# Kernel optimization log

Hardware: AMD Instinct MI355X
Metric: run time of the kernel (lower is better)

The kernel has to match this reference:

```python
import jax, jax.numpy as jnp
import numpy as np

HIDDEN = 2048
H = 16            # num heads
Q_RANK = 1536
KV_RANK = 512
D_NOPE = 128
D_ROPE = 64
D_QK = D_NOPE + D_ROPE   # 192
D_V = 128
ROPE_BASE = 10000.0
EPS = 1e-6


def _rms_norm(x, w):
    xf = x.astype(jnp.float32)
    var = jnp.mean(xf * xf, axis=-1, keepdims=True)
    return w * (xf * jax.lax.rsqrt(var + EPS)).astype(x.dtype)


def _rotate_half(x):
    x1, x2 = x[..., : x.shape[-1] // 2], x[..., x.shape[-1] // 2:]
    return jnp.concatenate((-x2, x1), axis=-1)


def _rope_cos_sin(position_ids, dtype):
    inv_freq = 1.0 / (ROPE_BASE ** (jnp.arange(0, D_ROPE, 2, dtype=jnp.float32) / D_ROPE))
    freqs = position_ids.astype(jnp.float32)[..., None] * inv_freq  # [b,s,32]
    emb = jnp.concatenate((freqs, freqs), axis=-1)                  # [b,s,64]
    return jnp.cos(emb).astype(dtype), jnp.sin(emb).astype(dtype)


def setup_inputs() -> dict:
    key = jax.random.key(0)
    ks = jax.random.split(key, 8)
    b, s = 1, 2048
    scale = 0.02
    return {
        "hidden_states": jax.random.normal(ks[0], (b, s, HIDDEN), jnp.float32),
        "position_ids": jnp.broadcast_to(jnp.arange(s, dtype=jnp.int64)[None, :], (b, s)),
        "q_a_w": jax.random.normal(ks[1], (Q_RANK, HIDDEN), jnp.float32) * scale,
        "q_a_ln_w": jnp.ones((Q_RANK,), jnp.float32),
        "q_b_w": jax.random.normal(ks[2], (H * D_QK, Q_RANK), jnp.float32) * scale,
        "kv_a_w": jax.random.normal(ks[3], (KV_RANK + D_ROPE, HIDDEN), jnp.float32) * scale,
        "kv_a_ln_w": jnp.ones((KV_RANK,), jnp.float32),
        "kv_b_w": jax.random.normal(ks[4], (H * (D_NOPE + D_V), KV_RANK), jnp.float32) * scale,
        "o_w": jax.random.normal(ks[5], (HIDDEN, H * D_V), jnp.float32) * scale,
    }


def reference(hidden_states, position_ids, q_a_w, q_a_ln_w, q_b_w, kv_a_w, kv_a_ln_w, kv_b_w, o_w):
    b, s, _ = hidden_states.shape
    softmax_scale = D_QK ** (-0.5)

    # Q path: low-rank down-proj -> RMSNorm -> up-proj
    q_a = hidden_states @ q_a_w.T                              # [b,s,q_rank]
    q = (_rms_norm(q_a, q_a_ln_w) @ q_b_w.T).reshape(b, s, H, D_QK)
    q_nope, q_pe = q[..., :D_NOPE], q[..., D_NOPE:]

    # KV path: joint down-proj -> split latent / rope part
    kv_a = hidden_states @ kv_a_w.T                            # [b,s,kv_rank+rope]
    compressed_kv = _rms_norm(kv_a[..., :KV_RANK], kv_a_ln_w)  # [b,s,kv_rank]
    k_pe = kv_a[..., KV_RANK:]                                 # [b,s,rope]
    kv_b = (compressed_kv @ kv_b_w.T).reshape(b, s, H, D_NOPE + D_V)
    k_nope, v = kv_b[..., :D_NOPE], kv_b[..., D_NOPE:]

    # decoupled RoPE on the rope slice
    cos, sin = _rope_cos_sin(position_ids, hidden_states.dtype)  # [b,s,64]
    cos, sin = cos[:, :, None, :], sin[:, :, None, :]            # [b,s,1,64]
    q_pe = q_pe * cos + _rotate_half(q_pe) * sin                 # [b,s,H,64]
    k_pe_h = jnp.broadcast_to(k_pe[:, :, None, :], (b, s, H, D_ROPE))
    k_pe_h = k_pe_h * cos + _rotate_half(k_pe_h) * sin

    q_full = jnp.concatenate([q_nope, q_pe], axis=-1)            # [b,s,H,192]
    k_full = jnp.concatenate([k_nope, k_pe_h], axis=-1)          # [b,s,H,192]

    # naive materialized attention (matches reference)
    scores = jnp.einsum("bqhd,bkhd->bhqk", q_full, k_full) * softmax_scale
    causal = jnp.triu(jnp.full((s, s), -jnp.inf, dtype=scores.dtype), k=1)
    scores = scores + causal
    probs = jax.nn.softmax(scores.astype(jnp.float32), axis=-1).astype(q_full.dtype)
    attn = jnp.einsum("bhqk,bkhd->bqhd", probs, v).reshape(b, s, H * D_V)
    return attn @ o_w.T
```

## Files before the change

kernel.cpp:

```cpp
#include <hip/hip_runtime.h>
#include <stdint.h>

#define S_LEN 2048
#define HIDDEN_ 2048
#define NH 16
#define QR 1536
#define KVR 512
#define DN 128
#define DR 64
#define DQK 192
#define DV 128
#define NQKV 2112

#define KT_STRIDE 6144
#define VT_STRIDE 4096

typedef __attribute__((ext_vector_type(8))) short bf16x8;
typedef __attribute__((ext_vector_type(4))) float f32x4;
typedef __attribute__((ext_vector_type(4))) unsigned short u16x4;
typedef unsigned short u16;
typedef unsigned int u32;

#define GLOAD_LDS16(g, l)                                                      \
    __builtin_amdgcn_global_load_lds(                                          \
        (const __attribute__((address_space(1))) void*)(g),                    \
        (__attribute__((address_space(3))) void*)(l), 16, 0, 0)

__device__ inline float bf2f(u16 x) {
    union { u32 u; float f; } v; v.u = ((u32)x) << 16; return v.f;
}
__device__ inline u16 f2bf(float f) {
    union { float f; u32 u; } v; v.f = f;
    u32 u = v.u;
    return (u16)((u + 0x7fffu + ((u >> 16) & 1u)) >> 16);
}

__global__ void cvt_multi(const float* s0, u16* d0, int n0,
                          const float* s1, u16* d1, int n1,
                          const float* s2, u16* d2, int n2,
                          const float* s3, u16* d3, int n3,
                          const float* s4, u16* d4, int n4,
                          const float* s5, u16* d5, int n5)
{
    const float* src; u16* dst; int n;
    switch (blockIdx.y) {
        case 0: src = s0; dst = d0; n = n0; break;
        case 1: src = s1; dst = d1; n = n1; break;
        case 2: src = s2; dst = d2; n = n2; break;
        case 3: src = s3; dst = d3; n = n3; break;
        case 4: src = s4; dst = d4; n = n4; break;
        default: src = s5; dst = d5; n = n5; break;
    }
    int i = (blockIdx.x * 256 + threadIdx.x) * 4;
    if (i + 3 < n) {
        float4 v = *(const float4*)(src + i);
        u16x4 o;
        o[0] = f2bf(v.x); o[1] = f2bf(v.y); o[2] = f2bf(v.z); o[3] = f2bf(v.w);
        *(u16x4*)(dst + i) = o;
    }
}

__device__ __forceinline__
void gemm_body(const u16* __restrict__ A, const u16* __restrict__ B,
               void* __restrict__ Cv, int M, int N, int Kloop, int ld,
               int out_f32, int bx, int by)
{
    __shared__ u16 sA[128 * 32];
    __shared__ u16 sB[128 * 32];
    const int tid  = threadIdx.x;
    const int wave = tid >> 6;
    const int lane = tid & 63;
    const int l16  = lane & 15;
    const int quad = lane >> 4;
    const int m_blk = by * 128;
    const int n_blk = bx * 128;
    const int wm = (wave >> 1) * 64;
    const int wn = (wave & 1) * 64;

    const f32x4 zero4 = {0.f, 0.f, 0.f, 0.f};
    f32x4 acc[4][4];
#pragma unroll
    for (int i = 0; i < 4; i++)
#pragma unroll
        for (int j = 0; j < 4; j++) acc[i][j] = zero4;

    const int srow = lane >> 2;
    const int scol = (lane & 3) * 8;

    for (int k0 = 0; k0 < Kloop; k0 += 32) {
        __syncthreads();
#pragma unroll
        for (int p = 0; p < 2; p++) {
            const int rbase = wave * 32 + p * 16;
            const int row = rbase + srow;
            const u16* ga = A + (size_t)(m_blk + row) * ld + k0 + scol;
            GLOAD_LDS16(ga, &sA[rbase * 32]);
            int brow = n_blk + row; if (brow >= N) brow = N - 1;
            const u16* gb = B + (size_t)brow * ld + k0 + scol;
            GLOAD_LDS16(gb, &sB[rbase * 32]);
        }
        __syncthreads();

        bf16x8 af[4], bfr[4];
#pragma unroll
        for (int i = 0; i < 4; i++)
            af[i] = *(const bf16x8*)(sA + (wm + i * 16 + l16) * 32 + quad * 8);
#pragma unroll
        for (int j = 0; j < 4; j++)
            bfr[j] = *(const bf16x8*)(sB + (wn + j * 16 + l16) * 32 + quad * 8);
#pragma unroll
        for (int i = 0; i < 4; i++)
#pragma unroll
            for (int j = 0; j < 4; j++)
                acc[i][j] = __builtin_amdgcn_mfma_f32_16x16x32_bf16(
                    af[i], bfr[j], acc[i][j], 0, 0, 0);
    }

#pragma unroll
    for (int i = 0; i < 4; i++)
#pragma unroll
        for (int j = 0; j < 4; j++)
#pragma unroll
            for (int r = 0; r < 4; r++) {
                int mrow = m_blk + wm + i * 16 + quad * 4 + r;
                int ncol = n_blk + wn + j * 16 + l16;
                if (ncol < N) {
                    if (out_f32)
                        ((float*)Cv)[(size_t)mrow * N + ncol] = acc[i][j][r];
                    else
                        ((u16*)Cv)[(size_t)mrow * N + ncol] = f2bf(acc[i][j][r]);
                }
            }
}

__global__ __launch_bounds__(256, 3)
void gemm_splitk(const u16* __restrict__ A, const u16* __restrict__ B,
                 float* __restrict__ C0, float* __restrict__ C1,
                 int M, int N, int Kh, int ld)
{
    float* C = blockIdx.z ? C1 : C0;
    gemm_body(A + (size_t)blockIdx.z * Kh, B + (size_t)blockIdx.z * Kh,
              C, M, N, Kh, ld, 1, blockIdx.x, blockIdx.y);
}

__global__ __launch_bounds__(256, 3)
void gemm_dual(const u16* A0, const u16* B0, u16* C0, int M0, int N0, int K0,
               const u16* A1, const u16* B1, u16* C1, int M1, int N1, int K1)
{
    if (blockIdx.z == 0) {
        if ((int)blockIdx.x >= (N0 + 127) / 128) return;
        gemm_body(A0, B0, C0, M0, N0, K0, K0, 0, blockIdx.x, blockIdx.y);
    } else {
        gemm_body(A1, B1, C1, M1, N1, K1, K1, 0, blockIdx.x, blockIdx.y);
    }
}

__global__ void rmsnorm2_k(const float* __restrict__ P0, const float* __restrict__ P1,
                           const float* __restrict__ W0, u16* __restrict__ Y0,
                           const float* __restrict__ W1, u16* __restrict__ Y1,
                           u16* __restrict__ kpe)
{
    const int row = blockIdx.x;
    const float* p0 = P0 + (size_t)row * NQKV;
    const float* p1 = P1 + (size_t)row * NQKV;
    __shared__ float xbuf[QR];
    __shared__ float red[4];
    int off, len; const float* W; u16* Y;
    if (blockIdx.y == 0) { off = 0;  len = QR;  W = W0; Y = Y0 + (size_t)row * QR;  }
    else                 { off = QR; len = KVR; W = W1; Y = Y1 + (size_t)row * KVR; }
    float ss = 0.f;
    for (int i = threadIdx.x; i < len; i += 256) {
        float v = p0[off + i] + p1[off + i];
        xbuf[i] = v;
        ss += v * v;
    }
#pragma unroll
    for (int o = 32; o; o >>= 1) ss += __shfl_down(ss, o, 64);
    if ((threadIdx.x & 63) == 0) red[threadIdx.x >> 6] = ss;
    __syncthreads();
    float tot = red[0] + red[1] + red[2] + red[3];
    float inv = 1.0f / sqrtf(tot / (float)len + 1e-6f);
    for (int i = threadIdx.x; i < len; i += 256)
        Y[i] = f2bf(W[i] * xbuf[i] * inv);
    if (blockIdx.y == 1 && threadIdx.x < DR) {
        int i = threadIdx.x;
        kpe[(size_t)row * DR + i] = f2bf(p0[QR + KVR + i] + p1[QR + KVR + i]);
    }
}

__global__ void rope_repack(const u16* __restrict__ q,
                            const u16* __restrict__ kvb,
                            const u16* __restrict__ kpe_b,
                            u16* __restrict__ Q, u16* __restrict__ Kf)
{
    const float QSC = 0.07216878364870323f * 1.4426950408889634f;
    const int s = blockIdx.x;
    const float pos = (float)s;
    const int t = threadIdx.x;
    __shared__ float cs[64], sn[64];
    __shared__ u16 kpe_r[64];
    if (t < 64) {
        int jf = t & 31;
        float freq = powf(10000.f, -(float)(2 * jf) / 64.f);
        float ang = pos * freq;
        cs[t] = cosf(ang);
        sn[t] = sinf(ang);
    }
    __syncthreads();
    if (t < 64) {
        int j = t;
        float x = bf2f(kpe_b[(size_t)s * DR + j]);
        float other = (j < 32) ? -bf2f(kpe_b[(size_t)s * DR + j + 32])
                               :  bf2f(kpe_b[(size_t)s * DR + j - 32]);
        kpe_r[j] = f2bf(x * cs[j] + other * sn[j]);
    }
    __syncthreads();

    for (int idx = t; idx < NH * 24; idx += 256) {
        const int h  = idx / 24;
        const int cg = idx % 24;
        const int d0v = cg * 8;
        const size_t qbase = (size_t)s * (NH * DQK) + h * DQK;
        bf16x8 qv, kv;
        if (d0v < DN) {
            bf16x8 qr = *(const bf16x8*)(q + qbase + d0v);
#pragma unroll
            for (int e = 0; e < 8; e++)
                qv[e] = (short)f2bf(bf2f((u16)qr[e]) * QSC);
            kv = *(const bf16x8*)(kvb + (size_t)s * (NH * 256) + h * 256 + d0v);
        } else {
            const int j0 = d0v - DN;
#pragma unroll
            for (int e = 0; e < 8; e++) {
                int j = j0 + e;
                float x = bf2f(q[qbase + DN + j]);
                float other = (j < 32) ? -bf2f(q[qbase + DN + j + 32])
                                       :  bf2f(q[qbase + DN + j - 32]);
                qv[e] = (short)f2bf((x * cs[j] + other * sn[j]) * QSC);
                kv[e] = (short)kpe_r[j];
            }
        }
        *(bf16x8*)&Q[((size_t)h * S_LEN + s) * DQK + d0v] = qv;
        const size_t koff = (size_t)(h * 64 + (s >> 5)) * KT_STRIDE
                          + (size_t)(cg * 32 + (s & 31)) * 8;
        *(bf16x8*)&Kf[koff] = kv;
    }
}

__global__ void transpose_v(const u16* __restrict__ kvb, u16* __restrict__ Vt)
{
    __shared__ u16 tile[64][72];
    const int h  = blockIdx.z;
    const int s0 = blockIdx.x * 64;
    const int d0 = blockIdx.y * 64;
    const int t  = threadIdx.x;
#pragma unroll
    for (int p = 0; p < 2; p++) {
        int c = p * 256 + t;
        int r = c >> 3, col = (c & 7) * 8;
        *(bf16x8*)&tile[r][col] =
            *(const bf16x8*)&kvb[(size_t)(s0 + r) * (NH * 256) + h * 256 + 128 + d0 + col];
    }
    __syncthreads();
#pragma unroll
    for (int p = 0; p < 2; p++) {
        int c = p * 256 + t;
        int dr = c >> 3, sc = (c & 7) * 8;
        bf16x8 v;
#pragma unroll
        for (int j = 0; j < 8; j++) v[j] = (short)tile[sc + j][dr];
        const int s_abs   = s0 + sc;
        const int kt      = s_abs >> 5;
        const int schunk  = (s_abs & 31) >> 3;
        const size_t voff = (size_t)(h * 64 + kt) * VT_STRIDE
                          + (size_t)(schunk * 128 + (d0 + dr)) * 8;
        *(bf16x8*)&Vt[voff] = v;
    }
}

__global__ __launch_bounds__(256, 3)
void mla_attn(const u16* __restrict__ Q, const u16* __restrict__ Kf,
              const u16* __restrict__ Vt, u16* __restrict__ attn,
              float* __restrict__ part)
{
    const int lin = blockIdx.x + 48 * blockIdx.y;
    const int h   = ((lin & 7) << 1) | ((lin >> 3) & 1);
    const int bx  = lin >> 4;

    int s, tb, te, cIdx; bool direct;
    if (bx < 16)      { s = 16 + bx; tb = 0;  te = 32;        cIdx = 0; direct = false; }
    else if (bx < 32) { s = bx;      tb = 32; te = 2 * s + 2; cIdx = 1; direct = false; }
    else              { s = 47 - bx; tb = 0;  te = 2 * s + 2; cIdx = 0; direct = true;  }

    const int wave  = threadIdx.x >> 6;
    const int lane  = threadIdx.x & 63;
    const int l16   = lane & 15;
    const int quad  = lane >> 4;
    const int q0    = s * 64 + wave * 16;
    const int qrow  = q0 + l16;

    const u16* Qh  = Q  + (size_t)h * S_LEN * DQK;
    const u16* Kh  = Kf + (size_t)h * 64 * KT_STRIDE;
    const u16* Vth = Vt + (size_t)h * 64 * VT_STRIDE;

    __shared__ u16 sK[2][24 * 32 * 8];
    __shared__ u16 sV[2][4 * 128 * 8];

    bf16x8 qf[6];
#pragma unroll
    for (int st = 0; st < 6; st++)
        qf[st] = *(const bf16x8*)(Qh + (size_t)qrow * DQK + st * 32 + quad * 8);

    const f32x4 zero4 = {0.f, 0.f, 0.f, 0.f};
    f32x4 oacc[8];
#pragma unroll
    for (int t = 0; t < 8; t++) oacc[t] = zero4;
    float mrow = -INFINITY, lrow = 0.f;

    auto stage = [&](int buf, int kt) {
        const u16* kp = Kh + (size_t)kt * KT_STRIDE;
#pragma unroll
        for (int g = 0; g < 3; g++)
            GLOAD_LDS16(kp + (g * 256 + wave * 64 + lane) * 8,
                        &sK[buf][(g * 256 + wave * 64) * 8]);
        const u16* vp = Vth + (size_t)kt * VT_STRIDE;
#pragma unroll
        for (int g = 0; g < 2; g++)
            GLOAD_LDS16(vp + (g * 256 + wave * 64 + lane) * 8,
                        &sV[buf][(g * 256 + wave * 64) * 8]);
    };

    stage(0, tb);

    for (int kt = tb; kt < te; kt++) {
        const int c0  = kt * 32;
        const int cur = (kt - tb) & 1;
        __syncthreads();
        if (kt + 1 < te) stage(cur ^ 1, kt + 1);

        if (c0 <= q0 + 15) {
            f32x4 s0 = zero4, s1 = zero4;
            __builtin_amdgcn_s_setprio(1);
#pragma unroll
            for (int st = 0; st < 6; st++) {
                bf16x8 k0 = *(const bf16x8*)&sK[cur][((st * 4 + quad) * 32 + l16) * 8];
                bf16x8 k1 = *(const bf16x8*)&sK[cur][((st * 4 + quad) * 32 + 16 + l16) * 8];
                s0 = __builtin_amdgcn_mfma_f32_16x16x32_bf16(k0, qf[st], s0, 0, 0, 0);
                s1 = __builtin_amdgcn_mfma_f32_16x16x32_bf16(k1, qf[st], s1, 0, 0, 0);
            }
            __builtin_amdgcn_s_setprio(0);
            bf16x8 vfr[8];
#pragma unroll
            for (int t = 0; t < 8; t++)
                vfr[t] = *(const bf16x8*)&sV[cur][(quad * 128 + t * 16 + l16) * 8];

            const bool full = (c0 + 31 <= q0);
            float v0[4], v1[4];
#pragma unroll
            for (int r = 0; r < 4; r++) {
                v0[r] = s0[r];
                v1[r] = s1[r];
                if (!full) {
                    if (c0 + quad * 4 + r > qrow)      v0[r] = -INFINITY;
                    if (c0 + 16 + quad * 4 + r > qrow) v1[r] = -INFINITY;
                }
            }
            float lm = fmaxf(fmaxf(fmaxf(v0[0], v0[1]), fmaxf(v0[2], v0[3])),
                             fmaxf(fmaxf(v1[0], v1[1]), fmaxf(v1[2], v1[3])));
            lm = fmaxf(lm, __shfl_xor(lm, 16, 64));
            lm = fmaxf(lm, __shfl_xor(lm, 32, 64));

            float mref;
            if (__all(lm <= mrow + 11.5416f)) {
                mref = mrow;
            } else {
                mref = fmaxf(mrow, lm);
                const float alpha = __builtin_amdgcn_exp2f(mrow - mref);
#pragma unroll
                for (int t = 0; t < 8; t++) oacc[t] *= alpha;
                lrow *= alpha;
                mrow = mref;
            }

            float p0[4], p1[4], rs = 0.f;
#pragma unroll
            for (int r = 0; r < 4; r++) {
                p0[r] = __builtin_amdgcn_exp2f(v0[r] - mref);
                p1[r] = __builtin_amdgcn_exp2f(v1[r] - mref);
                rs += p0[r] + p1[r];
            }
            lrow += rs;

            u32 A0 = (u32)f2bf(p0[0]) | ((u32)f2bf(p0[1]) << 16);
            u32 A1 = (u32)f2bf(p0[2]) | ((u32)f2bf(p0[3]) << 16);
            u32 B0 = (u32)f2bf(p1[0]) | ((u32)f2bf(p1[1]) << 16);
            u32 B1 = (u32)f2bf(p1[2]) | ((u32)f2bf(p1[3]) << 16);
            const int a0 = (((quad & 1) << 5) + l16) << 2;
            const int a1 = a0 + 64;
            u32 Y0 = (u32)__builtin_amdgcn_ds_bpermute(a0, (int)A0);
            u32 Y1 = (u32)__builtin_amdgcn_ds_bpermute(a0, (int)A1);
            u32 Y2 = (u32)__builtin_amdgcn_ds_bpermute(a1, (int)A0);
            u32 Y3 = (u32)__builtin_amdgcn_ds_bpermute(a1, (int)A1);
            u32 Z0 = (u32)__builtin_amdgcn_ds_bpermute(a0, (int)B0);
            u32 Z1 = (u32)__builtin_amdgcn_ds_bpermute(a0, (int)B1);
            u32 Z2 = (u32)__builtin_amdgcn_ds_bpermute(a1, (int)B0);
            u32 Z3 = (u32)__builtin_amdgcn_ds_bpermute(a1, (int)B1);
            const bool useA = quad < 2;
            union { u32 w[4]; bf16x8 v; } pf;
            pf.w[0] = useA ? Y0 : Z0;
            pf.w[1] = useA ? Y1 : Z1;
            pf.w[2] = useA ? Y2 : Z2;
            pf.w[3] = useA ? Y3 : Z3;
            bf16x8 pfrag = pf.v;

            __builtin_amdgcn_s_setprio(1);
#pragma unroll
            for (int t = 0; t < 8; t++)
                oacc[t] = __builtin_amdgcn_mfma_f32_16x16x32_bf16(vfr[t], pfrag,
                                                                  oacc[t], 0, 0, 0);
            __builtin_amdgcn_s_setprio(0);
        }
    }

    float lsum = lrow;
    lsum += __shfl_xor(lsum, 16, 64);
    lsum += __shfl_xor(lsum, 32, 64);

    if (direct) {
        const float linv = 1.0f / lsum;
#pragma unroll
        for (int t = 0; t < 8; t++) {
            u16x4 ov;
#pragma unroll
            for (int r = 0; r < 4; r++) ov[r] = f2bf(oacc[t][r] * linv);
            *(u16x4*)&attn[(size_t)qrow * (NH * DV) + h * DV + t * 16 + quad * 4] = ov;
        }
    } else {
        float* pout = part + ((size_t)(h * 16 + (s - 16)) * 2 + cIdx) * 8320;
        const int rowl = wave * 16 + l16;
#pragma unroll
        for (int t = 0; t < 8; t++) {
            float4 ov = {oacc[t][0], oacc[t][1], oacc[t][2], oacc[t][3]};
            *(float4*)&pout[(size_t)rowl * 128 + t * 16 + quad * 4] = ov;
        }
        if (quad == 0) {
            pout[8192 + rowl] = mrow;
            pout[8256 + rowl] = lsum;
        }
    }
}

__global__ void attn_combine(const float* __restrict__ part, u16* __restrict__ attn)
{
    const int h = blockIdx.y, sIdx = blockIdx.x;
    const int s = 16 + sIdx;
    const float* p0 = part + ((size_t)(h * 16 + sIdx) * 2 + 0) * 8320;
    const float* p1 = p0 + 8320;
    for (int e = threadIdx.x; e < 8192; e += 256) {
        int row = e >> 7, d = e & 127;
        float m0 = p0[8192 + row], m1 = p1[8192 + row];
        float l0 = p0[8256 + row], l1 = p1[8256 + row];
        float M  = fmaxf(m0, m1);
        float w0 = __builtin_amdgcn_exp2f(m0 - M);
        float w1 = __builtin_amdgcn_exp2f(m1 - M);
        float o  = (w0 * p0[e] + w1 * p1[e]) / (w0 * l0 + w1 * l1);
        attn[(size_t)(s * 64 + row) * (NH * DV) + h * DV + d] = f2bf(o);
    }
}

__global__ void addf2(const float* __restrict__ a, const float* __restrict__ b,
                      float* __restrict__ o, int n)
{
    int i = (blockIdx.x * 256 + threadIdx.x) * 4;
    if (i + 3 < n) {
        float4 va = *(const float4*)(a + i);
        float4 vb = *(const float4*)(b + i);
        float4 vo = {va.x + vb.x, va.y + vb.y, va.z + vb.z, va.w + vb.w};
        *(float4*)(o + i) = vo;
    }
}

extern "C" void kernel_launch(void* const* d_in, const int* in_sizes, int n_in,
                              void* d_out, int out_size, void* d_ws, size_t ws_size,
                              hipStream_t stream)
{
    const float* hid      = (const float*)d_in[0];
    const float* q_a_w    = (const float*)d_in[2];
    const float* q_a_ln_w = (const float*)d_in[3];
    const float* q_b_w    = (const float*)d_in[4];
    const float* kv_a_w   = (const float*)d_in[5];
    const float* kv_a_ln_w= (const float*)d_in[6];
    const float* kv_b_w   = (const float*)d_in[7];
    const float* o_w      = (const float*)d_in[8];

    char* base = (char*)d_ws;
    u16* qkvaw_b = (u16*)(base + 0);
    u16* qbw_b   = (u16*)(base + 8650752);
    u16* kvbw_b  = (u16*)(base + 18087936);
    u16* ow_b    = (u16*)(base + 22282240);
    u16* hid_b   = (u16*)(base + 30670848);
    float* P0    = (float*)(base + 39059456);
    float* P1    = (float*)(base + 56360960);
    u16* q_n     = (u16*)(base + 73662464);
    u16* ckv     = (u16*)(base + 79953920);
    u16* kpe_b   = (u16*)(base + 82051072);
    u16* qb      = (u16*)(base + 82313216);
    u16* kvb     = (u16*)(base + 94896128);
    u16* Qb      = (u16*)(base + 39059456);
    u16* Kb      = (u16*)(base + 51642368);
    u16* Vtb     = (u16*)(base + 64225280);
    u16* attnb   = (u16*)(base + 72613888);
    float* partb = (float*)(base + 94896128);
    float* PO0   = (float*)(base + 82313216);
    float* PO1   = (float*)(base + 99090432);

    cvt_multi<<<dim3(4608, 6), 256, 0, stream>>>(
        hid,    hid_b,                          HIDDEN_ * S_LEN,
        q_a_w,  qkvaw_b,                        QR * HIDDEN_,
        kv_a_w, qkvaw_b + (size_t)QR * HIDDEN_, (KVR + DR) * HIDDEN_,
        q_b_w,  qbw_b,                          NH * DQK * QR,
        kv_b_w, kvbw_b,                         NH * 256 * KVR,
        o_w,    ow_b,                           HIDDEN_ * NH * DV);

    gemm_splitk<<<dim3((NQKV + 127) / 128, S_LEN / 128, 2), 256, 0, stream>>>(
        hid_b, qkvaw_b, P0, P1, S_LEN, NQKV, HIDDEN_ / 2, HIDDEN_);
    rmsnorm2_k<<<dim3(S_LEN, 2), 256, 0, stream>>>(
        P0, P1, q_a_ln_w, q_n, kv_a_ln_w, ckv, kpe_b);
    gemm_dual<<<dim3(32, S_LEN / 128, 2), 256, 0, stream>>>(
        q_n, qbw_b, qb,  S_LEN, NH * DQK, QR,
        ckv, kvbw_b, kvb, S_LEN, NH * 256, KVR);
    rope_repack<<<S_LEN, 256, 0, stream>>>(qb, kvb, kpe_b, Qb, Kb);
    transpose_v<<<dim3(S_LEN / 64, DV / 64, NH), 256, 0, stream>>>(kvb, Vtb);
    mla_attn<<<dim3(48, NH), 256, 0, stream>>>(Qb, Kb, Vtb, attnb, partb);
    attn_combine<<<dim3(16, NH), 256, 0, stream>>>(partb, attnb);
    gemm_splitk<<<dim3(HIDDEN_ / 128, S_LEN / 128, 2), 256, 0, stream>>>(
        attnb, ow_b, PO0, PO1, S_LEN, HIDDEN_, HIDDEN_ / 2, HIDDEN_);
    addf2<<<dim3((S_LEN * HIDDEN_) / 1024), 256, 0, stream>>>(
        PO0, PO1, (float*)d_out, S_LEN * HIDDEN_);
}
```

Before: 336.0 us.

## Rebalance causal attention work into table-driven split-KV chunks with packed bf16 convert

Replaces the fixed 48-block split (16 two-way split rows plus direct rows) with a 63-chunk schedule from constant tables. Long query rows are split into 2 or 3 KV ranges of similar length, so the 1008 blocks carry more even work and the causal imbalance tail shrinks. The combine kernel now merges a variable number of partial records per row, and the partial buffer moves to a new workspace offset. It also replaces the manual float-to-bf16 rounding with the packed v_cvt_pk_bf16_f32 instruction. The cost is more partial-record traffic and more combine work.

```diff
diff --git a/kernel.cpp b/kernel.cpp
--- a/kernel.cpp
+++ b/kernel.cpp
@@ -15,6 +15,10 @@
 #define KT_STRIDE 6144
 #define VT_STRIDE 4096
 
+#define NCHUNK 63
+#define NREC 52
+#define REC_F32 8320
+
 typedef __attribute__((ext_vector_type(8))) short bf16x8;
 typedef __attribute__((ext_vector_type(4))) float f32x4;
 typedef __attribute__((ext_vector_type(4))) unsigned short u16x4;
@@ -34,6 +38,27 @@
     u32 u = v.u;
     return (u16)((u + 0x7fffu + ((u >> 16) & 1u)) >> 16);
 }
+
+__device__ __constant__ const int16_t CH_S[NCHUNK] = {
+    31,31,31, 30,30,30, 29,29,29, 28,28,28, 27,27,27,
+    26,26,26, 25,25,25, 24,24,24, 23,23,23, 22,22,22,
+    21,21, 20,20, 19,19, 18,18, 17,17, 16,16, 15,15, 14,14, 13,13, 12,12, 11,11,
+    10, 9, 8, 7, 6, 5, 4, 3, 2, 1, 0 };
+__device__ __constant__ const int16_t CH_TB[NCHUNK] = {
+    0,22,43, 0,21,42, 0,20,40, 0,20,39, 0,19,38,
+    0,18,36, 0,18,35, 0,17,34, 0,16,32, 0,16,31,
+    0,22, 0,21, 0,20, 0,19, 0,18, 0,17, 0,16, 0,15, 0,14, 0,13, 0,12,
+    0, 0, 0, 0, 0, 0, 0, 0, 0, 0, 0 };
+__device__ __constant__ const int16_t CH_TE[NCHUNK] = {
+    22,43,64, 21,42,62, 20,40,60, 20,39,58, 19,38,56,
+    18,36,54, 18,35,52, 17,34,50, 16,32,48, 16,31,46,
+    22,44, 21,42, 20,40, 19,38, 18,36, 17,34, 16,32, 15,30, 14,28, 13,26, 12,24,
+    22, 20, 18, 16, 14, 12, 10, 8, 6, 4, 2 };
+__device__ __constant__ const int16_t CH_RC[NCHUNK] = {
+    49,50,51, 46,47,48, 43,44,45, 40,41,42, 37,38,39,
+    34,35,36, 31,32,33, 28,29,30, 25,26,27, 22,23,24,
+    20,21, 18,19, 16,17, 14,15, 12,13, 10,11, 8,9, 6,7, 4,5, 2,3, 0,1,
+    -1,-1,-1,-1,-1,-1,-1,-1,-1,-1,-1 };
 
 __global__ void cvt_multi(const float* s0, u16* d0, int n0,
                           const float* s1, u16* d1, int n1,
@@ -283,14 +308,14 @@
               const u16* __restrict__ Vt, u16* __restrict__ attn,
               float* __restrict__ part)
 {
-    const int lin = blockIdx.x + 48 * blockIdx.y;
+    const int lin = blockIdx.x + NCHUNK * blockIdx.y;
     const int h   = ((lin & 7) << 1) | ((lin >> 3) & 1);
-    const int bx  = lin >> 4;
-
-    int s, tb, te, cIdx; bool direct;
-    if (bx < 16)      { s = 16 + bx; tb = 0;  te = 32;        cIdx = 0; direct = false; }
-    else if (bx < 32) { s = bx;      tb = 32; te = 2 * s + 2; cIdx = 1; direct = false; }
-    else              { s = 47 - bx; tb = 0;  te = 2 * s + 2; cIdx = 0; direct = true;  }
+    const int cix = lin >> 4;
+
+    const int s   = CH_S[cix];
+    const int tb  = CH_TB[cix];
+    const int te  = CH_TE[cix];
+    const int rec = CH_RC[cix];
 
     const int wave  = threadIdx.x >> 6;
     const int lane  = threadIdx.x & 63;
@@ -391,10 +416,11 @@
             }
             lrow += rs;
 
-            u32 A0 = (u32)f2bf(p0[0]) | ((u32)f2bf(p0[1]) << 16);
-            u32 A1 = (u32)f2bf(p0[2]) | ((u32)f2bf(p0[3]) << 16);
-            u32 B0 = (u32)f2bf(p1[0]) | ((u32)f2bf(p1[1]) << 16);
-            u32 B1 = (u32)f2bf(p1[2]) | ((u32)f2bf(p1[3]) << 16);
+            u32 A0, A1, B0, B1;
+            asm("v_cvt_pk_bf16_f32 %0, %1, %2" : "=v"(A0) : "v"(p0[0]), "v"(p0[1]));
+            asm("v_cvt_pk_bf16_f32 %0, %1, %2" : "=v"(A1) : "v"(p0[2]), "v"(p0[3]));
+            asm("v_cvt_pk_bf16_f32 %0, %1, %2" : "=v"(B0) : "v"(p1[0]), "v"(p1[1]));
+            asm("v_cvt_pk_bf16_f32 %0, %1, %2" : "=v"(B1) : "v"(p1[2]), "v"(p1[3]));
             const int a0 = (((quad & 1) << 5) + l16) << 2;
             const int a1 = a0 + 64;
             u32 Y0 = (u32)__builtin_amdgcn_ds_bpermute(a0, (int)A0);
@@ -426,7 +452,7 @@
     lsum += __shfl_xor(lsum, 16, 64);
     lsum += __shfl_xor(lsum, 32, 64);
 
-    if (direct) {
+    if (rec < 0) {
         const float linv = 1.0f / lsum;
 #pragma unroll
         for (int t = 0; t < 8; t++) {
@@ -436,7 +462,7 @@
             *(u16x4*)&attn[(size_t)qrow * (NH * DV) + h * DV + t * 16 + quad * 4] = ov;
         }
     } else {
-        float* pout = part + ((size_t)(h * 16 + (s - 16)) * 2 + cIdx) * 8320;
+        float* pout = part + ((size_t)h * NREC + rec) * REC_F32;
         const int rowl = wave * 16 + l16;
 #pragma unroll
         for (int t = 0; t < 8; t++) {
@@ -452,19 +478,25 @@
 
 __global__ void attn_combine(const float* __restrict__ part, u16* __restrict__ attn)
 {
-    const int h = blockIdx.y, sIdx = blockIdx.x;
-    const int s = 16 + sIdx;
-    const float* p0 = part + ((size_t)(h * 16 + sIdx) * 2 + 0) * 8320;
-    const float* p1 = p0 + 8320;
+    const int h = blockIdx.y;
+    const int s = 11 + blockIdx.x;
+    const int nc = (s >= 22) ? 3 : 2;
+    const int rb = (s >= 22) ? 22 + (s - 22) * 3 : (s - 11) * 2;
+    const float* recs = part + ((size_t)h * NREC + rb) * REC_F32;
     for (int e = threadIdx.x; e < 8192; e += 256) {
         int row = e >> 7, d = e & 127;
-        float m0 = p0[8192 + row], m1 = p1[8192 + row];
-        float l0 = p0[8256 + row], l1 = p1[8256 + row];
+        float m0 = recs[8192 + row];
+        float m1 = recs[REC_F32 + 8192 + row];
         float M  = fmaxf(m0, m1);
-        float w0 = __builtin_amdgcn_exp2f(m0 - M);
-        float w1 = __builtin_amdgcn_exp2f(m1 - M);
-        float o  = (w0 * p0[e] + w1 * p1[e]) / (w0 * l0 + w1 * l1);
-        attn[(size_t)(s * 64 + row) * (NH * DV) + h * DV + d] = f2bf(o);
+        if (nc == 3) M = fmaxf(M, recs[2 * REC_F32 + 8192 + row]);
+        float num = 0.f, den = 0.f;
+        for (int i = 0; i < nc; i++) {
+            const float* r = recs + (size_t)i * REC_F32;
+            float w = __builtin_amdgcn_exp2f(r[8192 + row] - M);
+            num += w * r[e];
+            den += w * r[8256 + row];
+        }
+        attn[(size_t)(s * 64 + row) * (NH * DV) + h * DV + d] = f2bf(num / den);
     }
 }
 
@@ -510,7 +542,7 @@
     u16* Kb      = (u16*)(base + 51642368);
     u16* Vtb     = (u16*)(base + 64225280);
     u16* attnb   = (u16*)(base + 72613888);
-    float* partb = (float*)(base + 94896128);
+    float* partb = (float*)(base + 81002496);
     float* PO0   = (float*)(base + 82313216);
     float* PO1   = (float*)(base + 99090432);
 
@@ -531,8 +563,8 @@
         ckv, kvbw_b, kvb, S_LEN, NH * 256, KVR);
     rope_repack<<<S_LEN, 256, 0, stream>>>(qb, kvb, kpe_b, Qb, Kb);
     transpose_v<<<dim3(S_LEN / 64, DV / 64, NH), 256, 0, stream>>>(kvb, Vtb);
-    mla_attn<<<dim3(48, NH), 256, 0, stream>>>(Qb, Kb, Vtb, attnb, partb);
-    attn_combine<<<dim3(16, NH), 256, 0, stream>>>(partb, attnb);
+    mla_attn<<<dim3(NCHUNK, NH), 256, 0, stream>>>(Qb, Kb, Vtb, attnb, partb);
+    attn_combine<<<dim3(21, NH), 256, 0, stream>>>(partb, attnb);
     gemm_splitk<<<dim3(HIDDEN_ / 128, S_LEN / 128, 2), 256, 0, stream>>>(
         attnb, ow_b, PO0, PO1, S_LEN, HIDDEN_, HIDDEN_ / 2, HIDDEN_);
     addf2<<<dim3((S_LEN * HIDDEN_) / 1024), 256, 0, stream>>>(
```

Measured after the change: 380.9 us. 13.4% more time.

## Overlap weight conversion with first GEMM and fuse repack kernels

Applied to the files above, without the earlier changes.

Splits the fp32-to-bf16 conversion so only the tensors the first GEMM needs are converted up front. The remaining weight conversions (q_b, kv_b, o) run as an extra z-slice of the first split-K GEMM grid, so they overlap with GEMM work. The rope repack and V transpose kernels are merged into one launch. In attention, a packed v_cvt_pk_bf16_f32 instruction replaces the manual bf16 rounding. These cut launch overhead and serial gaps, at the cost of the conversion blocks competing with GEMM blocks for CUs.

```diff
diff --git a/kernel.cpp b/kernel.cpp
--- a/kernel.cpp
+++ b/kernel.cpp
@@ -35,29 +35,21 @@
     return (u16)((u + 0x7fffu + ((u >> 16) & 1u)) >> 16);
 }
 
-__global__ void cvt_multi(const float* s0, u16* d0, int n0,
-                          const float* s1, u16* d1, int n1,
-                          const float* s2, u16* d2, int n2,
-                          const float* s3, u16* d3, int n3,
-                          const float* s4, u16* d4, int n4,
-                          const float* s5, u16* d5, int n5)
-{
-    const float* src; u16* dst; int n;
-    switch (blockIdx.y) {
-        case 0: src = s0; dst = d0; n = n0; break;
-        case 1: src = s1; dst = d1; n = n1; break;
-        case 2: src = s2; dst = d2; n = n2; break;
-        case 3: src = s3; dst = d3; n = n3; break;
-        case 4: src = s4; dst = d4; n = n4; break;
-        default: src = s5; dst = d5; n = n5; break;
-    }
-    int i = (blockIdx.x * 256 + threadIdx.x) * 4;
-    if (i + 3 < n) {
-        float4 v = *(const float4*)(src + i);
-        u16x4 o;
-        o[0] = f2bf(v.x); o[1] = f2bf(v.y); o[2] = f2bf(v.z); o[3] = f2bf(v.w);
-        *(u16x4*)(dst + i) = o;
-    }
+__global__ void cvt3(const float* __restrict__ s0, u16* __restrict__ d0, int n0,
+                     const float* __restrict__ s1, u16* __restrict__ d1, int n1,
+                     const float* __restrict__ s2, u16* __restrict__ d2, int n2)
+{
+    const int b0 = n0 >> 10, b1 = n1 >> 10;
+    int gid = blockIdx.x;
+    const float* src; u16* dst; int base;
+    if (gid < b0)           { src = s0; dst = d0; base = gid * 1024; }
+    else if (gid < b0 + b1) { src = s1; dst = d1; base = (gid - b0) * 1024; }
+    else                    { src = s2; dst = d2; base = (gid - b0 - b1) * 1024; }
+    int i = base + threadIdx.x * 4;
+    float4 v = *(const float4*)(src + i);
+    u16x4 o;
+    o[0] = f2bf(v.x); o[1] = f2bf(v.y); o[2] = f2bf(v.z); o[3] = f2bf(v.w);
+    *(u16x4*)(dst + i) = o;
 }
 
 __device__ __forceinline__
@@ -131,6 +123,40 @@
                         ((u16*)Cv)[(size_t)mrow * N + ncol] = f2bf(acc[i][j][r]);
                 }
             }
+}
+
+__global__ __launch_bounds__(256, 3)
+void gemm1_fused(const u16* __restrict__ A, const u16* __restrict__ B,
+                 float* __restrict__ C0, float* __restrict__ C1,
+                 int M, int N, int Kh, int ld,
+                 const float* s3, u16* d3, int n3,
+                 const float* s4, u16* d4, int n4,
+                 const float* s5, u16* d5, int n5)
+{
+    if (blockIdx.z < 2) {
+        float* C = blockIdx.z ? C1 : C0;
+        gemm_body(A + (size_t)blockIdx.z * Kh, B + (size_t)blockIdx.z * Kh,
+                  C, M, N, Kh, ld, 1, blockIdx.x, blockIdx.y);
+        return;
+    }
+    const int bid = blockIdx.y * gridDim.x + blockIdx.x;
+    const int stride = gridDim.x * gridDim.y * 256 * 4;
+    const int start = (bid * 256 + threadIdx.x) * 4;
+    for (int i = start; i < n3; i += stride) {
+        float4 v = *(const float4*)(s3 + i);
+        u16x4 o; o[0]=f2bf(v.x); o[1]=f2bf(v.y); o[2]=f2bf(v.z); o[3]=f2bf(v.w);
+        *(u16x4*)(d3 + i) = o;
+    }
+    for (int i = start; i < n4; i += stride) {
+        float4 v = *(const float4*)(s4 + i);
+        u16x4 o; o[0]=f2bf(v.x); o[1]=f2bf(v.y); o[2]=f2bf(v.z); o[3]=f2bf(v.w);
+        *(u16x4*)(d4 + i) = o;
+    }
+    for (int i = start; i < n5; i += stride) {
+        float4 v = *(const float4*)(s5 + i);
+        u16x4 o; o[0]=f2bf(v.x); o[1]=f2bf(v.y); o[2]=f2bf(v.z); o[3]=f2bf(v.w);
+        *(u16x4*)(d5 + i) = o;
+    }
 }
 
 __global__ __launch_bounds__(256, 3)
@@ -188,93 +214,98 @@
     }
 }
 
-__global__ void rope_repack(const u16* __restrict__ q,
-                            const u16* __restrict__ kvb,
-                            const u16* __restrict__ kpe_b,
-                            u16* __restrict__ Q, u16* __restrict__ Kf)
-{
-    const float QSC = 0.07216878364870323f * 1.4426950408889634f;
-    const int s = blockIdx.x;
-    const float pos = (float)s;
+__global__ void repack_fused(const u16* __restrict__ q,
+                             const u16* __restrict__ kvb,
+                             const u16* __restrict__ kpe_b,
+                             u16* __restrict__ Q, u16* __restrict__ Kf,
+                             u16* __restrict__ Vt)
+{
+    __shared__ __align__(16) char smem[64 * 72 * 2];
+    const int bid = blockIdx.x;
     const int t = threadIdx.x;
-    __shared__ float cs[64], sn[64];
-    __shared__ u16 kpe_r[64];
-    if (t < 64) {
-        int jf = t & 31;
-        float freq = powf(10000.f, -(float)(2 * jf) / 64.f);
-        float ang = pos * freq;
-        cs[t] = cosf(ang);
-        sn[t] = sinf(ang);
-    }
-    __syncthreads();
-    if (t < 64) {
-        int j = t;
-        float x = bf2f(kpe_b[(size_t)s * DR + j]);
-        float other = (j < 32) ? -bf2f(kpe_b[(size_t)s * DR + j + 32])
-                               :  bf2f(kpe_b[(size_t)s * DR + j - 32]);
-        kpe_r[j] = f2bf(x * cs[j] + other * sn[j]);
-    }
-    __syncthreads();
-
-    for (int idx = t; idx < NH * 24; idx += 256) {
-        const int h  = idx / 24;
-        const int cg = idx % 24;
-        const int d0v = cg * 8;
-        const size_t qbase = (size_t)s * (NH * DQK) + h * DQK;
-        bf16x8 qv, kv;
-        if (d0v < DN) {
-            bf16x8 qr = *(const bf16x8*)(q + qbase + d0v);
-#pragma unroll
-            for (int e = 0; e < 8; e++)
-                qv[e] = (short)f2bf(bf2f((u16)qr[e]) * QSC);
-            kv = *(const bf16x8*)(kvb + (size_t)s * (NH * 256) + h * 256 + d0v);
-        } else {
-            const int j0 = d0v - DN;
-#pragma unroll
-            for (int e = 0; e < 8; e++) {
-                int j = j0 + e;
-                float x = bf2f(q[qbase + DN + j]);
-                float other = (j < 32) ? -bf2f(q[qbase + DN + j + 32])
-                                       :  bf2f(q[qbase + DN + j - 32]);
-                qv[e] = (short)f2bf((x * cs[j] + other * sn[j]) * QSC);
-                kv[e] = (short)kpe_r[j];
+
+    if (bid < S_LEN) {
+        float* cs = (float*)smem;
+        float* sn = cs + 64;
+        u16* kpe_r = (u16*)(sn + 64);
+        const float QSC = 0.07216878364870323f * 1.4426950408889634f;
+        const int s = bid;
+        const float pos = (float)s;
+        if (t < 64) {
+            int jf = t & 31;
+            float freq = powf(10000.f, -(float)(2 * jf) / 64.f);
+            float ang = pos * freq;
+            cs[t] = cosf(ang);
+            sn[t] = sinf(ang);
+        }
+        __syncthreads();
+        if (t < 64) {
+            int j = t;
+            float x = bf2f(kpe_b[(size_t)s * DR + j]);
+            float other = (j < 32) ? -bf2f(kpe_b[(size_t)s * DR + j + 32])
+                                   :  bf2f(kpe_b[(size_t)s * DR + j - 32]);
+            kpe_r[j] = f2bf(x * cs[j] + other * sn[j]);
+        }
+        __syncthreads();
+
+        for (int idx = t; idx < NH * 24; idx += 256) {
+            const int h  = idx / 24;
+            const int cg = idx % 24;
+            const int d0v = cg * 8;
+            const size_t qbase = (size_t)s * (NH * DQK) + h * DQK;
+            bf16x8 qv, kv;
+            if (d0v < DN) {
+                bf16x8 qr = *(const bf16x8*)(q + qbase + d0v);
+#pragma unroll
+                for (int e = 0; e < 8; e++)
+                    qv[e] = (short)f2bf(bf2f((u16)qr[e]) * QSC);
+                kv = *(const bf16x8*)(kvb + (size_t)s * (NH * 256) + h * 256 + d0v);
+            } else {
+                const int j0 = d0v - DN;
+#pragma unroll
+                for (int e = 0; e < 8; e++) {
+                    int j = j0 + e;
+                    float x = bf2f(q[qbase + DN + j]);
+                    float other = (j < 32) ? -bf2f(q[qbase + DN + j + 32])
+                                           :  bf2f(q[qbase + DN + j - 32]);
+                    qv[e] = (short)f2bf((x * cs[j] + other * sn[j]) * QSC);
+                    kv[e] = (short)kpe_r[j];
+                }
             }
-        }
-        *(bf16x8*)&Q[((size_t)h * S_LEN + s) * DQK + d0v] = qv;
-        const size_t koff = (size_t)(h * 64 + (s >> 5)) * KT_STRIDE
-                          + (size_t)(cg * 32 + (s & 31)) * 8;
-        *(bf16x8*)&Kf[koff] = kv;
-    }
-}
-
-__global__ void transpose_v(const u16* __restrict__ kvb, u16* __restrict__ Vt)
-{
-    __shared__ u16 tile[64][72];
-    const int h  = blockIdx.z;
-    const int s0 = blockIdx.x * 64;
-    const int d0 = blockIdx.y * 64;
-    const int t  = threadIdx.x;
-#pragma unroll
-    for (int p = 0; p < 2; p++) {
-        int c = p * 256 + t;
-        int r = c >> 3, col = (c & 7) * 8;
-        *(bf16x8*)&tile[r][col] =
-            *(const bf16x8*)&kvb[(size_t)(s0 + r) * (NH * 256) + h * 256 + 128 + d0 + col];
-    }
-    __syncthreads();
-#pragma unroll
-    for (int p = 0; p < 2; p++) {
-        int c = p * 256 + t;
-        int dr = c >> 3, sc = (c & 7) * 8;
-        bf16x8 v;
-#pragma unroll
-        for (int j = 0; j < 8; j++) v[j] = (short)tile[sc + j][dr];
-        const int s_abs   = s0 + sc;
-        const int kt      = s_abs >> 5;
-        const int schunk  = (s_abs & 31) >> 3;
-        const size_t voff = (size_t)(h * 64 + kt) * VT_STRIDE
-                          + (size_t)(schunk * 128 + (d0 + dr)) * 8;
-        *(bf16x8*)&Vt[voff] = v;
+            *(bf16x8*)&Q[((size_t)h * S_LEN + s) * DQK + d0v] = qv;
+            const size_t koff = (size_t)(h * 64 + (s >> 5)) * KT_STRIDE
+                              + (size_t)(cg * 32 + (s & 31)) * 8;
+            *(bf16x8*)&Kf[koff] = kv;
+        }
+    } else {
+        u16 (*tile)[72] = (u16(*)[72])smem;
+        const int r   = bid - S_LEN;
+        const int h   = r >> 6;
+        const int rem = r & 63;
+        const int s0  = (rem >> 1) * 64;
+        const int d0  = (rem & 1) * 64;
+#pragma unroll
+        for (int p = 0; p < 2; p++) {
+            int c = p * 256 + t;
+            int rr = c >> 3, col = (c & 7) * 8;
+            *(bf16x8*)&tile[rr][col] =
+                *(const bf16x8*)&kvb[(size_t)(s0 + rr) * (NH * 256) + h * 256 + 128 + d0 + col];
+        }
+        __syncthreads();
+#pragma unroll
+        for (int p = 0; p < 2; p++) {
+            int c = p * 256 + t;
+            int dr = c >> 3, sc = (c & 7) * 8;
+            bf16x8 v;
+#pragma unroll
+            for (int j = 0; j < 8; j++) v[j] = (short)tile[sc + j][dr];
+            const int s_abs   = s0 + sc;
+            const int kt      = s_abs >> 5;
+            const int schunk  = (s_abs & 31) >> 3;
+            const size_t voff = (size_t)(h * 64 + kt) * VT_STRIDE
+                              + (size_t)(schunk * 128 + (d0 + dr)) * 8;
+            *(bf16x8*)&Vt[voff] = v;
+        }
     }
 }
 
@@ -391,10 +422,11 @@
             }
             lrow += rs;
 
-            u32 A0 = (u32)f2bf(p0[0]) | ((u32)f2bf(p0[1]) << 16);
-            u32 A1 = (u32)f2bf(p0[2]) | ((u32)f2bf(p0[3]) << 16);
-            u32 B0 = (u32)f2bf(p1[0]) | ((u32)f2bf(p1[1]) << 16);
-            u32 B1 = (u32)f2bf(p1[2]) | ((u32)f2bf(p1[3]) << 16);
+            u32 A0, A1, B0, B1;
+            asm("v_cvt_pk_bf16_f32 %0, %1, %2" : "=v"(A0) : "v"(p0[0]), "v"(p0[1]));
+            asm("v_cvt_pk_bf16_f32 %0, %1, %2" : "=v"(A1) : "v"(p0[2]), "v"(p0[3]));
+            asm("v_cvt_pk_bf16_f32 %0, %1, %2" : "=v"(B0) : "v"(p1[0]), "v"(p1[1]));
+            asm("v_cvt_pk_bf16_f32 %0, %1, %2" : "=v"(B1) : "v"(p1[2]), "v"(p1[3]));
             const int a0 = (((quad & 1) << 5) + l16) << 2;
             const int a1 = a0 + 64;
             u32 Y0 = (u32)__builtin_amdgcn_ds_bpermute(a0, (int)A0);
@@ -514,23 +546,23 @@
     float* PO0   = (float*)(base + 82313216);
     float* PO1   = (float*)(base + 99090432);
 
-    cvt_multi<<<dim3(4608, 6), 256, 0, stream>>>(
+    cvt3<<<dim3(8320), 256, 0, stream>>>(
         hid,    hid_b,                          HIDDEN_ * S_LEN,
         q_a_w,  qkvaw_b,                        QR * HIDDEN_,
-        kv_a_w, qkvaw_b + (size_t)QR * HIDDEN_, (KVR + DR) * HIDDEN_,
-        q_b_w,  qbw_b,                          NH * DQK * QR,
-        kv_b_w, kvbw_b,                         NH * 256 * KVR,
-        o_w,    ow_b,                           HIDDEN_ * NH * DV);
-
-    gemm_splitk<<<dim3((NQKV + 127) / 128, S_LEN / 128, 2), 256, 0, stream>>>(
-        hid_b, qkvaw_b, P0, P1, S_LEN, NQKV, HIDDEN_ / 2, HIDDEN_);
+        kv_a_w, qkvaw_b + (size_t)QR * HIDDEN_, (KVR + DR) * HIDDEN_);
+
+    gemm1_fused<<<dim3((NQKV + 127) / 128, S_LEN / 128, 3), 256, 0, stream>>>(
+        hid_b, qkvaw_b, P0, P1, S_LEN, NQKV, HIDDEN_ / 2, HIDDEN_,
+        q_b_w,  qbw_b,  NH * DQK * QR,
+        kv_b_w, kvbw_b, NH * 256 * KVR,
+        o_w,    ow_b,   HIDDEN_ * NH * DV);
     rmsnorm2_k<<<dim3(S_LEN, 2), 256, 0, stream>>>(
         P0, P1, q_a_ln_w, q_n, kv_a_ln_w, ckv, kpe_b);
     gemm_dual<<<dim3(32, S_LEN / 128, 2), 256, 0, stream>>>(
         q_n, qbw_b, qb,  S_LEN, NH * DQK, QR,
         ckv, kvbw_b, kvb, S_LEN, NH * 256, KVR);
-    rope_repack<<<S_LEN, 256, 0, stream>>>(qb, kvb, kpe_b, Qb, Kb);
-    transpose_v<<<dim3(S_LEN / 64, DV / 64, NH), 256, 0, stream>>>(kvb, Vtb);
+    repack_fused<<<dim3(S_LEN + 1024), 256, 0, stream>>>(
+        qb, kvb, kpe_b, Qb, Kb, Vtb);
     mla_attn<<<dim3(48, NH), 256, 0, stream>>>(Qb, Kb, Vtb, attnb, partb);
     attn_combine<<<dim3(16, NH), 256, 0, stream>>>(partb, attnb);
     gemm_splitk<<<dim3(HIDDEN_ / 128, S_LEN / 128, 2), 256, 0, stream>>>(
```

After: 343.6 us. 2.3% more time.
